# Kernel optimization log

Measured on AMD Instinct MI355X. Metric: run time of the kernel, lower is better.

## Reference

```python
import jax, jax.numpy as jnp
import numpy as np
import math

D_MODEL = 512
N_HEADS = 8
BMIN, BMAX = 0.3, 1.0
W_E, W_M, W_I = 0.4, 0.4, 0.2


def norm_minmax(t):
    t_min = t.min(axis=-1, keepdims=True)
    t_max = t.max(axis=-1, keepdims=True)
    return (t - t_min) / jnp.maximum(t_max - t_min, 1e-8)


def setup_inputs() -> dict:
    key = jax.random.key(0)
    ks = jax.random.split(key, 12)
    B, S, D, C = 2, 2048, D_MODEL, 1000
    x = jax.random.normal(ks[0], (B, S, D), dtype=jnp.float32)
    out_probs = jax.nn.softmax(jax.random.normal(ks[1], (B, C), dtype=jnp.float32), axis=-1)
    idf_seq = jax.random.uniform(ks[2], (B, S), dtype=jnp.float32)
    def lin(kw, kb):
        W = jax.random.normal(kw, (D, D), dtype=jnp.float32) * 0.02
        b = jax.random.normal(kb, (D,), dtype=jnp.float32) * 0.02
        return W, b
    Wq, bq = lin(ks[3], ks[4])
    Wk, bk = lin(ks[5], ks[6])
    Wv, bv = lin(ks[7], ks[8])
    Wo, bo = lin(ks[9], ks[10])
    return dict(x=x, out_probs=out_probs, idf_seq=idf_seq,
                Wq=Wq, bq=bq, Wk=Wk, bk=bk, Wv=Wv, bv=bv, Wo=Wo, bo=bo)


def reference(x, out_probs, idf_seq, Wq, bq, Wk, bk, Wv, bv, Wo, bo):
    B, S, D = x.shape
    H = N_HEADS
    dk = D // H

    def heads(W, b):
        # (B,S,D) -> (B,H,S,dk)
        return (x @ W.T + b).reshape(B, S, H, dk).swapaxes(1, 2)

    q = heads(Wq, bq)
    k = heads(Wk, bk)
    v = heads(Wv, bv)

    logits = jnp.einsum('bhqd,bhkd->bhqk', q, k) / math.sqrt(dk)
    attn_probs = jax.nn.softmax(logits, axis=-1)  # (B,H,S,S)

    # --- compute_load ---
    p = jnp.maximum(attn_probs, 1e-12)
    H_i = (-(p * jnp.log(p)).sum(axis=-1)).mean(axis=1)  # (B,S)
    H_i = norm_minmax(H_i)

    top2 = jax.lax.top_k(out_probs, 2)[0]  # (B,2)
    margin = jnp.maximum(top2[:, 0] - top2[:, 1], 0.0)[:, None]  # (B,1)
    margin = jnp.broadcast_to(margin, (B, S))
    margin = norm_minmax(margin)
    load_from_margin = 1.0 - margin

    L = W_E * H_i + W_M * load_from_margin + W_I * idf_seq
    L = norm_minmax(L)

    # --- map load to budget and cap ---
    Bgt = BMIN + (BMAX - BMIN) * L  # (B,S)
    row_sum = jnp.maximum(attn_probs.sum(axis=-1, keepdims=True), 1e-12)  # (B,H,S,1)
    scale = jnp.minimum(Bgt[:, None, :, None] / row_sum, 1.0)
    attn_probs = attn_probs * scale

    y = jnp.einsum('bhqk,bhkd->bhqd', attn_probs, v)  # (B,H,S,dk)
    y = y.swapaxes(1, 2).reshape(B, S, D)
    y = y @ Wo.T + bo
    return y, attn_probs
```

## Files before the change

### kernel.cpp

```cpp
#include <hip/hip_runtime.h>
#include <hip/hip_bf16.h>


typedef __attribute__((ext_vector_type(8))) short bf16x8;
typedef __attribute__((ext_vector_type(4))) float f32x4;

static __device__ __forceinline__ unsigned short f2b(float f) {
  union { float f; unsigned int u; } v; v.f = f;
  unsigned int u = v.u;
  u += 0x7FFF + ((u >> 16) & 1);
  return (unsigned short)(u >> 16);
}

__global__ __launch_bounds__(256) void cvt_all(
    const float* __restrict__ x,
    const float* __restrict__ Wq, const float* __restrict__ Wk,
    const float* __restrict__ Wv, const float* __restrict__ Wo,
    unsigned short* __restrict__ xb, unsigned short* __restrict__ wqkv,
    unsigned short* __restrict__ wob)
{
  int i = blockIdx.x * 256 + threadIdx.x;
  const float* s; unsigned short* d; int off;
  if (i < 524288) { s = x; d = xb; off = i; }
  else {
    int j = i - 524288; int w = j >> 16; off = j & 65535;
    switch (w) {
      case 0: s = Wq; d = wqkv; break;
      case 1: s = Wk; d = wqkv + 262144; break;
      case 2: s = Wv; d = wqkv + 524288; break;
      default: s = Wo; d = wob; break;
    }
  }
  float4 v = reinterpret_cast<const float4*>(s)[off];
  ushort4 o;
  o.x = f2b(v.x); o.y = f2b(v.y); o.z = f2b(v.z); o.w = f2b(v.w);
  reinterpret_cast<ushort4*>(d)[off] = o;
}

__global__ __launch_bounds__(256) void qkv_gemm(
    const unsigned short* __restrict__ xb, const unsigned short* __restrict__ w,
    const float* __restrict__ bq, const float* __restrict__ bk, const float* __restrict__ bv,
    unsigned short* __restrict__ Qb, unsigned short* __restrict__ Kb,
    unsigned short* __restrict__ Vtb)
{
  __shared__ unsigned short smem[5120];
  unsigned short* shA = smem;
  unsigned short* shB = smem + 2560;
  const int tid = threadIdx.x;
  const int bm = blockIdx.x, bn = blockIdx.y;
  const int lane = tid & 63, wid = tid >> 6;
  const int wr = wid >> 1, wc = wid & 1;
  const int lg = lane >> 4, lc = lane & 15;

  f32x4 acc[2][2];
#pragma unroll
  for (int i = 0; i < 2; ++i)
#pragma unroll
    for (int j = 0; j < 2; ++j) acc[i][j] = f32x4{0.f, 0.f, 0.f, 0.f};

  const int row_st = tid >> 2;
  const int k8 = (tid & 3) * 8;
  for (int kt = 0; kt < 16; ++kt) {
    *reinterpret_cast<uint4*>(&shA[row_st * 40 + k8]) =
        *reinterpret_cast<const uint4*>(&xb[(size_t)(bm * 64 + row_st) * 512 + kt * 32 + k8]);
    *reinterpret_cast<uint4*>(&shB[row_st * 40 + k8]) =
        *reinterpret_cast<const uint4*>(&w[(size_t)(bn * 64 + row_st) * 512 + kt * 32 + k8]);
    __syncthreads();
    bf16x8 af[2], bfr[2];
#pragma unroll
    for (int f = 0; f < 2; ++f) {
      af[f]  = *reinterpret_cast<const bf16x8*>(&shA[(wr * 32 + f * 16 + lc) * 40 + lg * 8]);
      bfr[f] = *reinterpret_cast<const bf16x8*>(&shB[(wc * 32 + f * 16 + lc) * 40 + lg * 8]);
    }
#pragma unroll
    for (int fm = 0; fm < 2; ++fm)
#pragma unroll
      for (int fn = 0; fn < 2; ++fn)
        acc[fm][fn] = __builtin_amdgcn_mfma_f32_16x16x32_bf16(af[fm], bfr[fn], acc[fm][fn], 0, 0, 0);
    __syncthreads();
  }

  if (bn < 16) {
#pragma unroll
    for (int fm = 0; fm < 2; ++fm)
#pragma unroll
      for (int fn = 0; fn < 2; ++fn)
#pragma unroll
        for (int r = 0; r < 4; ++r) {
          int mi = bm * 64 + wr * 32 + fm * 16 + lg * 4 + r;
          int ni = bn * 64 + wc * 32 + fn * 16 + lc;
          int bb = mi >> 11, s = mi & 2047;
          float v = acc[fm][fn][r];
          if (ni < 512) {
            int h = ni >> 6, d = ni & 63;
            v = (v + bq[ni]) * 0.125f;
            Qb[(((size_t)bb * 8 + h) * 2048 + s) * 64 + d] = f2b(v);
          } else {
            int i2 = ni - 512; int h = i2 >> 6, d = i2 & 63;
            v += bk[i2];
            Kb[(((size_t)bb * 8 + h) * 2048 + s) * 64 + d] = f2b(v);
          }
        }
  } else {
    unsigned short (*T)[80] = reinterpret_cast<unsigned short(*)[80]>(smem);
    __syncthreads();
#pragma unroll
    for (int fm = 0; fm < 2; ++fm)
#pragma unroll
      for (int fn = 0; fn < 2; ++fn)
#pragma unroll
        for (int r = 0; r < 4; ++r) {
          int nl = wc * 32 + fn * 16 + lc;
          int ml = wr * 32 + fm * 16 + lg * 4 + r;
          int i2 = (bn - 16) * 64 + nl;
          T[nl][ml] = f2b(acc[fm][fn][r] + bv[i2]);
        }
    __syncthreads();
    const int row = tid >> 3;
    const int seg = tid & 7;
    const int h = bn - 16;
    int mi = bm * 64 + seg * 8;
    int bb = mi >> 11, s = mi & 2047;
#pragma unroll
    for (int rr = 0; rr < 2; ++rr) {
      int d = row + rr * 32;
      *reinterpret_cast<uint4*>(&Vtb[(((size_t)bb * 8 + h) * 64 + d) * 2048 + s]) =
          *reinterpret_cast<const uint4*>(&T[d][seg * 8]);
    }
  }
}

__global__ __launch_bounds__(256) void attn_pass1(
    const unsigned short* __restrict__ Qb, const unsigned short* __restrict__ Kb,
    float* __restrict__ zA, float* __restrict__ tA)
{
  __shared__ unsigned short Kbuf[2][4096];
  const int l = blockIdx.x;
  const int l2 = (l & 7) * 64 + (l >> 3);
  const int bh = l2 >> 5;
  const int qt = l2 & 31;
  const int tid = threadIdx.x;
  const int lane = tid & 63, wid = tid >> 6;
  const int lg = lane >> 4, lc = lane & 15;
  const int q0 = qt * 64 + wid * 16;
  const unsigned short* Qp = Qb + (size_t)bh * 2048 * 64;
  const unsigned short* Kp = Kb + (size_t)bh * 2048 * 64;
  bf16x8 aq0 = *reinterpret_cast<const bf16x8*>(&Qp[(q0 + lc) * 64 + lg * 8]);
  bf16x8 aq1 = *reinterpret_cast<const bf16x8*>(&Qp[(q0 + lc) * 64 + lg * 8 + 32]);

  const int srow = tid >> 3;
  const int sseg = tid & 7;
  const int wIdx0 = (srow * 64 + sseg * 8) ^ ((srow & 7) << 3);
  const int wIdx1 = wIdx0 + 2048;
  const int rswz = (lc & 7) << 3;

  float Z_[4], T_[4];
#pragma unroll
  for (int r = 0; r < 4; ++r) { Z_[r] = 0.f; T_[r] = 0.f; }

  {
    uint4 g0 = *reinterpret_cast<const uint4*>(&Kp[(size_t)srow * 64 + sseg * 8]);
    uint4 g1 = *reinterpret_cast<const uint4*>(&Kp[(size_t)(srow + 32) * 64 + sseg * 8]);
    *reinterpret_cast<uint4*>(&Kbuf[0][wIdx0]) = g0;
    *reinterpret_cast<uint4*>(&Kbuf[0][wIdx1]) = g1;
    __syncthreads();
  }

  for (int t = 0; t < 32; ++t) {
    uint4 g0, g1;
    if (t < 31) {
      g0 = *reinterpret_cast<const uint4*>(&Kp[(size_t)((t + 1) * 64 + srow) * 64 + sseg * 8]);
      g1 = *reinterpret_cast<const uint4*>(&Kp[(size_t)((t + 1) * 64 + srow + 32) * 64 + sseg * 8]);
    }
    const unsigned short* kb = Kbuf[t & 1];
    f32x4 acc[4];
#pragma unroll
    for (int c = 0; c < 4; ++c) {
      int rI = (c * 16 + lc) * 64;
      bf16x8 b0 = *reinterpret_cast<const bf16x8*>(&kb[(rI + lg * 8) ^ rswz]);
      bf16x8 b1 = *reinterpret_cast<const bf16x8*>(&kb[(rI + 32 + lg * 8) ^ rswz]);
      f32x4 z = {0.f, 0.f, 0.f, 0.f};
      z = __builtin_amdgcn_mfma_f32_16x16x32_bf16(aq0, b0, z, 0, 0, 0);
      acc[c] = __builtin_amdgcn_mfma_f32_16x16x32_bf16(aq1, b1, z, 0, 0, 0);
    }
#pragma unroll
    for (int r = 0; r < 4; ++r) {
#pragma unroll
      for (int c = 0; c < 4; ++c) {
        float lv = acc[c][r];
        float e = __expf(lv);
        Z_[r] += e;
        T_[r] = fmaf(lv, e, T_[r]);
      }
    }
    if (t < 31) {
      *reinterpret_cast<uint4*>(&Kbuf[(t + 1) & 1][wIdx0]) = g0;
      *reinterpret_cast<uint4*>(&Kbuf[(t + 1) & 1][wIdx1]) = g1;
    }
    __syncthreads();
  }
#pragma unroll
  for (int r = 0; r < 4; ++r) {
#pragma unroll
    for (int msk = 1; msk < 16; msk <<= 1) {
      Z_[r] += __shfl_xor(Z_[r], msk);
      T_[r] += __shfl_xor(T_[r], msk);
    }
  }
  if (lc == 0) {
#pragma unroll
    for (int r = 0; r < 4; ++r) {
      int idx = bh * 2048 + q0 + lg * 4 + r;
      zA[idx] = Z_[r]; tA[idx] = T_[r];
    }
  }
}

__global__ __launch_bounds__(256) void load_kernel(
    const float* __restrict__ zA, const float* __restrict__ tA,
    const float* __restrict__ idf, float* __restrict__ scaleArr)
{
  const int b = blockIdx.x, t = threadIdx.x;
  __shared__ float sh[2048];
  __shared__ float rmin[256], rmax[256];
  for (int s = t; s < 2048; s += 256) {
    float acc = 0.f;
    for (int h = 0; h < 8; ++h) {
      int idx = (b * 8 + h) * 2048 + s;
      float Z = zA[idx];
      acc += logf(Z) - tA[idx] / Z;
    }
    sh[s] = acc * 0.125f;
  }
  __syncthreads();
  float mn = 3e38f, mx = -3e38f;
  for (int s = t; s < 2048; s += 256) { float v = sh[s]; mn = fminf(mn, v); mx = fmaxf(mx, v); }
  rmin[t] = mn; rmax[t] = mx; __syncthreads();
  for (int o = 128; o > 0; o >>= 1) {
    if (t < o) { rmin[t] = fminf(rmin[t], rmin[t + o]); rmax[t] = fmaxf(rmax[t], rmax[t + o]); }
    __syncthreads();
  }
  float Hmin = rmin[0], Hmax = rmax[0];
  __syncthreads();
  for (int s = t; s < 2048; s += 256) {
    float Hn = (sh[s] - Hmin) / fmaxf(Hmax - Hmin, 1e-8f);
    sh[s] = 0.4f * Hn + 0.4f + 0.2f * idf[b * 2048 + s];
  }
  __syncthreads();
  mn = 3e38f; mx = -3e38f;
  for (int s = t; s < 2048; s += 256) { float v = sh[s]; mn = fminf(mn, v); mx = fmaxf(mx, v); }
  rmin[t] = mn; rmax[t] = mx; __syncthreads();
  for (int o = 128; o > 0; o >>= 1) {
    if (t < o) { rmin[t] = fminf(rmin[t], rmin[t + o]); rmax[t] = fmaxf(rmax[t], rmax[t + o]); }
    __syncthreads();
  }
  float Lmin = rmin[0], Lmax = rmax[0];
  for (int s = t; s < 2048; s += 256) {
    float Ln = (sh[s] - Lmin) / fmaxf(Lmax - Lmin, 1e-8f);
    scaleArr[b * 2048 + s] = fminf(0.3f + 0.7f * Ln, 1.0f);
  }
}

__global__ __launch_bounds__(256) void attn_pass2(
    const unsigned short* __restrict__ Qb, const unsigned short* __restrict__ Kb,
    const unsigned short* __restrict__ Vtb,
    const float* __restrict__ zA, const float* __restrict__ scaleArr,
    float* __restrict__ attnOut, unsigned short* __restrict__ yh)
{
  __shared__ unsigned short Kbuf[2][4096];
  __shared__ unsigned short Vbuf[2][4096];
  __shared__ unsigned short Pb[4][16 * 72];
  const int l = blockIdx.x;
  const int l2 = (l & 7) * 64 + (l >> 3);
  const int bh = l2 >> 5;
  const int qt = l2 & 31;
  const int b = bh >> 3; const int h = bh & 7;
  const int tid = threadIdx.x;
  const int lane = tid & 63, wid = tid >> 6;
  const int lg = lane >> 4, lc = lane & 15;
  const int q0 = qt * 64 + wid * 16;
  const unsigned short* Qp = Qb + (size_t)bh * 2048 * 64;
  const unsigned short* Kp = Kb + (size_t)bh * 2048 * 64;
  const unsigned short* Vp = Vtb + (size_t)bh * 64 * 2048;
  bf16x8 aq0 = *reinterpret_cast<const bf16x8*>(&Qp[(q0 + lc) * 64 + lg * 8]);
  bf16x8 aq1 = *reinterpret_cast<const bf16x8*>(&Qp[(q0 + lc) * 64 + lg * 8 + 32]);
  float coef[4];
#pragma unroll
  for (int r = 0; r < 4; ++r) {
    int q = q0 + lg * 4 + r;
    coef[r] = scaleArr[b * 2048 + q] / zA[bh * 2048 + q];
  }
  f32x4 accY[4];
#pragma unroll
  for (int i = 0; i < 4; ++i) accY[i] = f32x4{0.f, 0.f, 0.f, 0.f};
  unsigned short* myP = Pb[wid];
  float* aBase = attnOut + (size_t)bh * 2048 * 2048;

  const int srow = tid >> 3, sseg = tid & 7;
  const int wIdx0 = (srow * 64 + sseg * 8) ^ ((srow & 7) << 3);
  const int wIdx1 = wIdx0 + 2048;
  const int rswz = (lc & 7) << 3;

  {
    uint4 k0_ = *reinterpret_cast<const uint4*>(&Kp[(size_t)srow * 64 + sseg * 8]);
    uint4 k1_ = *reinterpret_cast<const uint4*>(&Kp[(size_t)(srow + 32) * 64 + sseg * 8]);
    uint4 v0_ = *reinterpret_cast<const uint4*>(&Vp[(size_t)srow * 2048 + sseg * 8]);
    uint4 v1_ = *reinterpret_cast<const uint4*>(&Vp[(size_t)(srow + 32) * 2048 + sseg * 8]);
    *reinterpret_cast<uint4*>(&Kbuf[0][wIdx0]) = k0_;
    *reinterpret_cast<uint4*>(&Kbuf[0][wIdx1]) = k1_;
    *reinterpret_cast<uint4*>(&Vbuf[0][wIdx0]) = v0_;
    *reinterpret_cast<uint4*>(&Vbuf[0][wIdx1]) = v1_;
    __syncthreads();
  }

  for (int t = 0; t < 32; ++t) {
    uint4 gk0, gk1, gv0, gv1;
    if (t < 31) {
      int kn = (t + 1) * 64;
      gk0 = *reinterpret_cast<const uint4*>(&Kp[(size_t)(kn + srow) * 64 + sseg * 8]);
      gk1 = *reinterpret_cast<const uint4*>(&Kp[(size_t)(kn + srow + 32) * 64 + sseg * 8]);
      gv0 = *reinterpret_cast<const uint4*>(&Vp[(size_t)srow * 2048 + kn + sseg * 8]);
      gv1 = *reinterpret_cast<const uint4*>(&Vp[(size_t)(srow + 32) * 2048 + kn + sseg * 8]);
    }
    const unsigned short* kb = Kbuf[t & 1];
    const unsigned short* vb = Vbuf[t & 1];
    f32x4 acc[4];
#pragma unroll
    for (int c = 0; c < 4; ++c) {
      int rI = (c * 16 + lc) * 64;
      bf16x8 b0 = *reinterpret_cast<const bf16x8*>(&kb[(rI + lg * 8) ^ rswz]);
      bf16x8 b1 = *reinterpret_cast<const bf16x8*>(&kb[(rI + 32 + lg * 8) ^ rswz]);
      f32x4 z = {0.f, 0.f, 0.f, 0.f};
      z = __builtin_amdgcn_mfma_f32_16x16x32_bf16(aq0, b0, z, 0, 0, 0);
      acc[c] = __builtin_amdgcn_mfma_f32_16x16x32_bf16(aq1, b1, z, 0, 0, 0);
    }
#pragma unroll
    for (int c = 0; c < 4; ++c)
#pragma unroll
      for (int r = 0; r < 4; ++r) {
        float pv = __expf(acc[c][r]) * coef[r];
        myP[(lg * 4 + r) * 72 + c * 16 + lc] = f2b(pv);
      }
    const int k0g = t * 64;
#pragma unroll
    for (int j = 0; j < 4; ++j) {
      int row = j * 4 + lg;
      ushort4 p4 = *reinterpret_cast<const ushort4*>(&myP[row * 72 + lc * 4]);
      f32x4 v;
      v[0] = __uint_as_float((unsigned)p4.x << 16);
      v[1] = __uint_as_float((unsigned)p4.y << 16);
      v[2] = __uint_as_float((unsigned)p4.z << 16);
      v[3] = __uint_as_float((unsigned)p4.w << 16);
      *reinterpret_cast<f32x4*>(&aBase[(size_t)(q0 + row) * 2048 + k0g + lc * 4]) = v;
    }
#pragma unroll
    for (int kk = 0; kk < 2; ++kk) {
      bf16x8 ap = *reinterpret_cast<const bf16x8*>(&myP[lc * 72 + kk * 32 + lg * 8]);
#pragma unroll
      for (int cf = 0; cf < 4; ++cf) {
        int rI = (cf * 16 + lc) * 64;
        bf16x8 bv_ = *reinterpret_cast<const bf16x8*>(&vb[(rI + kk * 32 + lg * 8) ^ rswz]);
        accY[cf] = __builtin_amdgcn_mfma_f32_16x16x32_bf16(ap, bv_, accY[cf], 0, 0, 0);
      }
    }
    if (t < 31) {
      *reinterpret_cast<uint4*>(&Kbuf[(t + 1) & 1][wIdx0]) = gk0;
      *reinterpret_cast<uint4*>(&Kbuf[(t + 1) & 1][wIdx1]) = gk1;
      *reinterpret_cast<uint4*>(&Vbuf[(t + 1) & 1][wIdx0]) = gv0;
      *reinterpret_cast<uint4*>(&Vbuf[(t + 1) & 1][wIdx1]) = gv1;
    }
    __syncthreads();
  }
#pragma unroll
  for (int cf = 0; cf < 4; ++cf)
#pragma unroll
    for (int r = 0; r < 4; ++r) {
      int qrow = q0 + lg * 4 + r;
      yh[((size_t)b * 2048 + qrow) * 512 + h * 64 + cf * 16 + lc] = f2b(accY[cf][r]);
    }
}

__global__ __launch_bounds__(256) void out_gemm(
    const unsigned short* __restrict__ yhb, const unsigned short* __restrict__ wo,
    const float* __restrict__ bo, float* __restrict__ yOut)
{
  __shared__ unsigned short shA[64 * 40];
  __shared__ unsigned short shB[64 * 40];
  const int tid = threadIdx.x;
  const int bm = blockIdx.x, bn = blockIdx.y;
  const int lane = tid & 63, wid = tid >> 6;
  const int wr = wid >> 1, wc = wid & 1;
  const int lg = lane >> 4, lc = lane & 15;

  f32x4 acc[2][2];
#pragma unroll
  for (int i = 0; i < 2; ++i)
#pragma unroll
    for (int j = 0; j < 2; ++j) acc[i][j] = f32x4{0.f, 0.f, 0.f, 0.f};

  const int row_st = tid >> 2;
  const int k8 = (tid & 3) * 8;
  for (int kt = 0; kt < 16; ++kt) {
    *reinterpret_cast<uint4*>(&shA[row_st * 40 + k8]) =
        *reinterpret_cast<const uint4*>(&yhb[(size_t)(bm * 64 + row_st) * 512 + kt * 32 + k8]);
    *reinterpret_cast<uint4*>(&shB[row_st * 40 + k8]) =
        *reinterpret_cast<const uint4*>(&wo[(size_t)(bn * 64 + row_st) * 512 + kt * 32 + k8]);
    __syncthreads();
    bf16x8 af[2], bfr[2];
#pragma unroll
    for (int f = 0; f < 2; ++f) {
      af[f]  = *reinterpret_cast<const bf16x8*>(&shA[(wr * 32 + f * 16 + lc) * 40 + lg * 8]);
      bfr[f] = *reinterpret_cast<const bf16x8*>(&shB[(wc * 32 + f * 16 + lc) * 40 + lg * 8]);
    }
#pragma unroll
    for (int fm = 0; fm < 2; ++fm)
#pragma unroll
      for (int fn = 0; fn < 2; ++fn)
        acc[fm][fn] = __builtin_amdgcn_mfma_f32_16x16x32_bf16(af[fm], bfr[fn], acc[fm][fn], 0, 0, 0);
    __syncthreads();
  }
#pragma unroll
  for (int fm = 0; fm < 2; ++fm)
#pragma unroll
    for (int fn = 0; fn < 2; ++fn)
#pragma unroll
      for (int r = 0; r < 4; ++r) {
        int mi = bm * 64 + wr * 32 + fm * 16 + lg * 4 + r;
        int ni = bn * 64 + wc * 32 + fn * 16 + lc;
        yOut[(size_t)mi * 512 + ni] = acc[fm][fn][r] + bo[ni];
      }
}

extern "C" void kernel_launch(void* const* d_in, const int* in_sizes, int n_in,
                              void* d_out, int out_size, void* d_ws, size_t ws_size,
                              hipStream_t stream) {
  const float* x   = (const float*)d_in[0];
  const float* idf = (const float*)d_in[2];
  const float* Wq = (const float*)d_in[3];
  const float* bq = (const float*)d_in[4];
  const float* Wk = (const float*)d_in[5];
  const float* bk = (const float*)d_in[6];
  const float* Wv = (const float*)d_in[7];
  const float* bv = (const float*)d_in[8];
  const float* Wo = (const float*)d_in[9];
  const float* bo = (const float*)d_in[10];

  float* yOut = (float*)d_out;
  float* attnOut = yOut + (size_t)2 * 2048 * 512;

  char* p = (char*)d_ws;
  auto alloc = [&](size_t bytes) { char* r = p; p += (bytes + 255) & ~(size_t)255; return r; };
  unsigned short* xb   = (unsigned short*)alloc((size_t)2097152 * 2);
  unsigned short* wqkv = (unsigned short*)alloc((size_t)786432 * 2);
  unsigned short* wob  = (unsigned short*)alloc((size_t)262144 * 2);
  unsigned short* Qb   = (unsigned short*)alloc((size_t)2097152 * 2);
  unsigned short* Kb   = (unsigned short*)alloc((size_t)2097152 * 2);
  unsigned short* Vtb  = (unsigned short*)alloc((size_t)2097152 * 2);
  unsigned short* yh   = (unsigned short*)alloc((size_t)2097152 * 2);
  float* zA = (float*)alloc((size_t)32768 * 4);
  float* tA = (float*)alloc((size_t)32768 * 4);
  float* scaleArr = (float*)alloc((size_t)4096 * 4);

  cvt_all<<<3072, 256, 0, stream>>>(x, Wq, Wk, Wv, Wo, xb, wqkv, wob);
  qkv_gemm<<<dim3(64, 24), 256, 0, stream>>>(xb, wqkv, bq, bk, bv, Qb, Kb, Vtb);
  attn_pass1<<<512, 256, 0, stream>>>(Qb, Kb, zA, tA);
  load_kernel<<<2, 256, 0, stream>>>(zA, tA, idf, scaleArr);
  attn_pass2<<<512, 256, 0, stream>>>(Qb, Kb, Vtb, zA, scaleArr, attnOut, yh);
  out_gemm<<<dim3(64, 8), 256, 0, stream>>>(yh, wob, bo, yOut);
}
```

Measured before the change: 128.9 us.

## Split attention key range across two blocks to double grid parallelism

Both attention passes now launch 1024 blocks instead of 512, and each block handles half of the key sequence. Partial softmax sums and entropy terms are written per half and combined in the load kernel, which also stores the combined normaliser. The PV partial outputs go to two fp32 buffers that the output GEMM sums and converts to bf16 while loading. The aim is better occupancy on the many CUs, at the cost of extra fp32 partial-output traffic and a larger workspace.

```diff
diff --git a/kernel.cpp b/kernel.cpp
--- a/kernel.cpp
+++ b/kernel.cpp
@@ -136,9 +136,11 @@
 {
   __shared__ unsigned short Kbuf[2][4096];
   const int l = blockIdx.x;
-  const int l2 = (l & 7) * 64 + (l >> 3);
-  const int bh = l2 >> 5;
-  const int qt = l2 & 31;
+  const int l2 = (l & 7) * 128 + (l >> 3);
+  const int bh = l2 >> 6;
+  const int rem = l2 & 63;
+  const int qt = rem >> 1;
+  const int kh = rem & 1;
   const int tid = threadIdx.x;
   const int lane = tid & 63, wid = tid >> 6;
   const int lg = lane >> 4, lc = lane & 15;
@@ -153,24 +155,26 @@
   const int wIdx0 = (srow * 64 + sseg * 8) ^ ((srow & 7) << 3);
   const int wIdx1 = wIdx0 + 2048;
   const int rswz = (lc & 7) << 3;
+  const int kbase = kh * 16;
 
   float Z_[4], T_[4];
 #pragma unroll
   for (int r = 0; r < 4; ++r) { Z_[r] = 0.f; T_[r] = 0.f; }
 
   {
-    uint4 g0 = *reinterpret_cast<const uint4*>(&Kp[(size_t)srow * 64 + sseg * 8]);
-    uint4 g1 = *reinterpret_cast<const uint4*>(&Kp[(size_t)(srow + 32) * 64 + sseg * 8]);
+    uint4 g0 = *reinterpret_cast<const uint4*>(&Kp[(size_t)(kbase * 64 + srow) * 64 + sseg * 8]);
+    uint4 g1 = *reinterpret_cast<const uint4*>(&Kp[(size_t)(kbase * 64 + srow + 32) * 64 + sseg * 8]);
     *reinterpret_cast<uint4*>(&Kbuf[0][wIdx0]) = g0;
     *reinterpret_cast<uint4*>(&Kbuf[0][wIdx1]) = g1;
     __syncthreads();
   }
 
-  for (int t = 0; t < 32; ++t) {
+  for (int t = 0; t < 16; ++t) {
     uint4 g0, g1;
-    if (t < 31) {
-      g0 = *reinterpret_cast<const uint4*>(&Kp[(size_t)((t + 1) * 64 + srow) * 64 + sseg * 8]);
-      g1 = *reinterpret_cast<const uint4*>(&Kp[(size_t)((t + 1) * 64 + srow + 32) * 64 + sseg * 8]);
+    if (t < 15) {
+      int kn = (kbase + t + 1) * 64;
+      g0 = *reinterpret_cast<const uint4*>(&Kp[(size_t)(kn + srow) * 64 + sseg * 8]);
+      g1 = *reinterpret_cast<const uint4*>(&Kp[(size_t)(kn + srow + 32) * 64 + sseg * 8]);
     }
     const unsigned short* kb = Kbuf[t & 1];
     f32x4 acc[4];
@@ -193,7 +197,7 @@
         T_[r] = fmaf(lv, e, T_[r]);
       }
     }
-    if (t < 31) {
+    if (t < 15) {
       *reinterpret_cast<uint4*>(&Kbuf[(t + 1) & 1][wIdx0]) = g0;
       *reinterpret_cast<uint4*>(&Kbuf[(t + 1) & 1][wIdx1]) = g1;
     }
@@ -210,7 +214,7 @@
   if (lc == 0) {
 #pragma unroll
     for (int r = 0; r < 4; ++r) {
-      int idx = bh * 2048 + q0 + lg * 4 + r;
+      int idx = kh * 32768 + bh * 2048 + q0 + lg * 4 + r;
       zA[idx] = Z_[r]; tA[idx] = T_[r];
     }
   }
@@ -218,7 +222,8 @@
 
 __global__ __launch_bounds__(256) void load_kernel(
     const float* __restrict__ zA, const float* __restrict__ tA,
-    const float* __restrict__ idf, float* __restrict__ scaleArr)
+    const float* __restrict__ idf, float* __restrict__ scaleArr,
+    float* __restrict__ zC)
 {
   const int b = blockIdx.x, t = threadIdx.x;
   __shared__ float sh[2048];
@@ -227,8 +232,10 @@
     float acc = 0.f;
     for (int h = 0; h < 8; ++h) {
       int idx = (b * 8 + h) * 2048 + s;
-      float Z = zA[idx];
-      acc += logf(Z) - tA[idx] / Z;
+      float Z = zA[idx] + zA[idx + 32768];
+      float T = tA[idx] + tA[idx + 32768];
+      zC[idx] = Z;
+      acc += logf(Z) - T / Z;
     }
     sh[s] = acc * 0.125f;
   }
@@ -264,16 +271,18 @@
 __global__ __launch_bounds__(256) void attn_pass2(
     const unsigned short* __restrict__ Qb, const unsigned short* __restrict__ Kb,
     const unsigned short* __restrict__ Vtb,
-    const float* __restrict__ zA, const float* __restrict__ scaleArr,
-    float* __restrict__ attnOut, unsigned short* __restrict__ yh)
+    const float* __restrict__ zC, const float* __restrict__ scaleArr,
+    float* __restrict__ attnOut, float* __restrict__ yacc)
 {
   __shared__ unsigned short Kbuf[2][4096];
   __shared__ unsigned short Vbuf[2][4096];
   __shared__ unsigned short Pb[4][16 * 72];
   const int l = blockIdx.x;
-  const int l2 = (l & 7) * 64 + (l >> 3);
-  const int bh = l2 >> 5;
-  const int qt = l2 & 31;
+  const int l2 = (l & 7) * 128 + (l >> 3);
+  const int bh = l2 >> 6;
+  const int rem = l2 & 63;
+  const int qt = rem >> 1;
+  const int kh = rem & 1;
   const int b = bh >> 3; const int h = bh & 7;
   const int tid = threadIdx.x;
   const int lane = tid & 63, wid = tid >> 6;
@@ -288,7 +297,7 @@
 #pragma unroll
   for (int r = 0; r < 4; ++r) {
     int q = q0 + lg * 4 + r;
-    coef[r] = scaleArr[b * 2048 + q] / zA[bh * 2048 + q];
+    coef[r] = scaleArr[b * 2048 + q] / zC[bh * 2048 + q];
   }
   f32x4 accY[4];
 #pragma unroll
@@ -300,12 +309,14 @@
   const int wIdx0 = (srow * 64 + sseg * 8) ^ ((srow & 7) << 3);
   const int wIdx1 = wIdx0 + 2048;
   const int rswz = (lc & 7) << 3;
+  const int kbase = kh * 16;
 
   {
-    uint4 k0_ = *reinterpret_cast<const uint4*>(&Kp[(size_t)srow * 64 + sseg * 8]);
-    uint4 k1_ = *reinterpret_cast<const uint4*>(&Kp[(size_t)(srow + 32) * 64 + sseg * 8]);
-    uint4 v0_ = *reinterpret_cast<const uint4*>(&Vp[(size_t)srow * 2048 + sseg * 8]);
-    uint4 v1_ = *reinterpret_cast<const uint4*>(&Vp[(size_t)(srow + 32) * 2048 + sseg * 8]);
+    int kn = kbase * 64;
+    uint4 k0_ = *reinterpret_cast<const uint4*>(&Kp[(size_t)(kn + srow) * 64 + sseg * 8]);
+    uint4 k1_ = *reinterpret_cast<const uint4*>(&Kp[(size_t)(kn + srow + 32) * 64 + sseg * 8]);
+    uint4 v0_ = *reinterpret_cast<const uint4*>(&Vp[(size_t)srow * 2048 + kn + sseg * 8]);
+    uint4 v1_ = *reinterpret_cast<const uint4*>(&Vp[(size_t)(srow + 32) * 2048 + kn + sseg * 8]);
     *reinterpret_cast<uint4*>(&Kbuf[0][wIdx0]) = k0_;
     *reinterpret_cast<uint4*>(&Kbuf[0][wIdx1]) = k1_;
     *reinterpret_cast<uint4*>(&Vbuf[0][wIdx0]) = v0_;
@@ -313,10 +324,10 @@
     __syncthreads();
   }
 
-  for (int t = 0; t < 32; ++t) {
+  for (int t = 0; t < 16; ++t) {
     uint4 gk0, gk1, gv0, gv1;
-    if (t < 31) {
-      int kn = (t + 1) * 64;
+    if (t < 15) {
+      int kn = (kbase + t + 1) * 64;
       gk0 = *reinterpret_cast<const uint4*>(&Kp[(size_t)(kn + srow) * 64 + sseg * 8]);
       gk1 = *reinterpret_cast<const uint4*>(&Kp[(size_t)(kn + srow + 32) * 64 + sseg * 8]);
       gv0 = *reinterpret_cast<const uint4*>(&Vp[(size_t)srow * 2048 + kn + sseg * 8]);
@@ -341,7 +352,7 @@
         float pv = __expf(acc[c][r]) * coef[r];
         myP[(lg * 4 + r) * 72 + c * 16 + lc] = f2b(pv);
       }
-    const int k0g = t * 64;
+    const int k0g = (kbase + t) * 64;
 #pragma unroll
     for (int j = 0; j < 4; ++j) {
       int row = j * 4 + lg;
@@ -363,7 +374,7 @@
         accY[cf] = __builtin_amdgcn_mfma_f32_16x16x32_bf16(ap, bv_, accY[cf], 0, 0, 0);
       }
     }
-    if (t < 31) {
+    if (t < 15) {
       *reinterpret_cast<uint4*>(&Kbuf[(t + 1) & 1][wIdx0]) = gk0;
       *reinterpret_cast<uint4*>(&Kbuf[(t + 1) & 1][wIdx1]) = gk1;
       *reinterpret_cast<uint4*>(&Vbuf[(t + 1) & 1][wIdx0]) = gv0;
@@ -371,17 +382,18 @@
     }
     __syncthreads();
   }
+  float* yH = yacc + (size_t)kh * 2097152;
 #pragma unroll
   for (int cf = 0; cf < 4; ++cf)
 #pragma unroll
     for (int r = 0; r < 4; ++r) {
       int qrow = q0 + lg * 4 + r;
-      yh[((size_t)b * 2048 + qrow) * 512 + h * 64 + cf * 16 + lc] = f2b(accY[cf][r]);
+      yH[((size_t)b * 2048 + qrow) * 512 + h * 64 + cf * 16 + lc] = accY[cf][r];
     }
 }
 
 __global__ __launch_bounds__(256) void out_gemm(
-    const unsigned short* __restrict__ yhb, const unsigned short* __restrict__ wo,
+    const float* __restrict__ yacc, const unsigned short* __restrict__ wo,
     const float* __restrict__ bo, float* __restrict__ yOut)
 {
   __shared__ unsigned short shA[64 * 40];
@@ -400,9 +412,20 @@
 
   const int row_st = tid >> 2;
   const int k8 = (tid & 3) * 8;
+  const size_t mBase = (size_t)(bm * 64 + row_st) * 512;
   for (int kt = 0; kt < 16; ++kt) {
-    *reinterpret_cast<uint4*>(&shA[row_st * 40 + k8]) =
-        *reinterpret_cast<const uint4*>(&yhb[(size_t)(bm * 64 + row_st) * 512 + kt * 32 + k8]);
+    const float* y0 = &yacc[mBase + kt * 32 + k8];
+    const float* y1 = y0 + 2097152;
+    float4 a0 = *reinterpret_cast<const float4*>(y0);
+    float4 a1 = *reinterpret_cast<const float4*>(y0 + 4);
+    float4 c0 = *reinterpret_cast<const float4*>(y1);
+    float4 c1 = *reinterpret_cast<const float4*>(y1 + 4);
+    uint4 pk;
+    pk.x = (unsigned)f2b(a0.x + c0.x) | ((unsigned)f2b(a0.y + c0.y) << 16);
+    pk.y = (unsigned)f2b(a0.z + c0.z) | ((unsigned)f2b(a0.w + c0.w) << 16);
+    pk.z = (unsigned)f2b(a1.x + c1.x) | ((unsigned)f2b(a1.y + c1.y) << 16);
+    pk.w = (unsigned)f2b(a1.z + c1.z) | ((unsigned)f2b(a1.w + c1.w) << 16);
+    *reinterpret_cast<uint4*>(&shA[row_st * 40 + k8]) = pk;
     *reinterpret_cast<uint4*>(&shB[row_st * 40 + k8]) =
         *reinterpret_cast<const uint4*>(&wo[(size_t)(bn * 64 + row_st) * 512 + kt * 32 + k8]);
     __syncthreads();
@@ -456,15 +479,16 @@
   unsigned short* Qb   = (unsigned short*)alloc((size_t)2097152 * 2);
   unsigned short* Kb   = (unsigned short*)alloc((size_t)2097152 * 2);
   unsigned short* Vtb  = (unsigned short*)alloc((size_t)2097152 * 2);
-  unsigned short* yh   = (unsigned short*)alloc((size_t)2097152 * 2);
-  float* zA = (float*)alloc((size_t)32768 * 4);
-  float* tA = (float*)alloc((size_t)32768 * 4);
+  float* yacc = (float*)alloc((size_t)4194304 * 4);
+  float* zA = (float*)alloc((size_t)65536 * 4);
+  float* tA = (float*)alloc((size_t)65536 * 4);
+  float* zCc = (float*)alloc((size_t)32768 * 4);
   float* scaleArr = (float*)alloc((size_t)4096 * 4);
 
   cvt_all<<<3072, 256, 0, stream>>>(x, Wq, Wk, Wv, Wo, xb, wqkv, wob);
   qkv_gemm<<<dim3(64, 24), 256, 0, stream>>>(xb, wqkv, bq, bk, bv, Qb, Kb, Vtb);
-  attn_pass1<<<512, 256, 0, stream>>>(Qb, Kb, zA, tA);
-  load_kernel<<<2, 256, 0, stream>>>(zA, tA, idf, scaleArr);
-  attn_pass2<<<512, 256, 0, stream>>>(Qb, Kb, Vtb, zA, scaleArr, attnOut, yh);
-  out_gemm<<<dim3(64, 8), 256, 0, stream>>>(yh, wob, bo, yOut);
-}
+  attn_pass1<<<1024, 256, 0, stream>>>(Qb, Kb, zA, tA);
+  load_kernel<<<2, 256, 0, stream>>>(zA, tA, idf, scaleArr, zCc);
+  attn_pass2<<<1024, 256, 0, stream>>>(Qb, Kb, Vtb, zCc, scaleArr, attnOut, yacc);
+  out_gemm<<<dim3(64, 8), 256, 0, stream>>>(yacc, wob, bo, yOut);
+}
```

New measurement: 134.3 us. 4.2% more time.
